# Optimization experiments

Hardware: AMD Instinct MI355X
Metric: run time of the kernel (lower is better)

Reference implementation:

```python
import jax, jax.numpy as jnp
import numpy as np

SAMPLING = 16   # VGG16 feature stride
POOL = 7        # adaptive max pool output size
KMAX = 5        # max bin window; valid for ROI feature extents <= 28 cells
NEG = jnp.float32(-1e30)


def _bin_bounds(s0, L, i):
    # torch AdaptiveMaxPool2d bin i over a length-L crop starting at s0:
    # [s0 + floor(i*L/P), s0 + ceil((i+1)*L/P))
    bs = s0 + (i * L) // POOL
    be = s0 + ((i + 1) * L + POOL - 1) // POOL
    return bs, be


def setup_inputs() -> dict:
    key = jax.random.key(0)
    ks = jax.random.split(key, 12)
    N, C, Hf, Wf = 1024, 512, 50, 84
    Himg, Wimg = Hf * SAMPLING, Wf * SAMPLING
    # post-ReLU VGG features -> non-negative
    featmap = jax.random.uniform(ks[0], (1, C, Hf, Wf), dtype=jnp.float32)
    # ROI boxes [x0, y0, x1, y1] in pixel coords, extents in [32, 448] px
    x0 = jax.random.randint(ks[1], (N,), 0, Wimg - 448)
    y0 = jax.random.randint(ks[2], (N,), 0, Himg - 448)
    w = jax.random.randint(ks[3], (N,), 32, 449)
    h = jax.random.randint(ks[4], (N,), 32, 449)
    roi = jnp.stack([x0, y0, x0 + w, y0 + h], axis=1).astype(jnp.int32)
    d = C * POOL * POOL  # 25088
    W1 = jax.random.normal(ks[5], (d, 4096), dtype=jnp.float32) * 0.01
    b1 = jnp.zeros((4096,), jnp.float32)
    W2 = jax.random.normal(ks[6], (4096, 4096), dtype=jnp.float32) * 0.01
    b2 = jnp.zeros((4096,), jnp.float32)
    Wc = jax.random.normal(ks[7], (4096, 3), dtype=jnp.float32) * 0.01
    bc = jnp.zeros((3,), jnp.float32)
    Wr = jax.random.normal(ks[8], (4096, 12), dtype=jnp.float32) * 0.01
    br = jnp.zeros((12,), jnp.float32)
    return {"featmap": featmap, "roi": roi, "W1": W1, "b1": b1, "W2": W2,
            "b2": b2, "Wc": Wc, "bc": bc, "Wr": Wr, "br": br}


def _roipool(featmap, roi):
    fm = featmap[0]                       # (C, Hf, Wf)
    C, Hf, Wf = fm.shape
    rf = roi // SAMPLING                  # floor, coords are non-negative
    x0, y0, x1, y1 = rf[:, 0], rf[:, 1], rf[:, 2], rf[:, 3]
    # width expand: if x1-x0 <= 1 -> grow right if in-bounds else grow left
    nw = (x1 - x0) <= 1
    x0n = jnp.where(nw & ~(x1 < Wf), x0 - 1, x0)
    x1n = jnp.where(nw & (x1 < Wf), x1 + 1, x1)
    nh = (y1 - y0) <= 1
    y0n = jnp.where(nh & ~(y1 < Hf), y0 - 1, y0)
    y1n = jnp.where(nh & (y1 < Hf), y1 + 1, y1)
    # python slice semantics clamp to array bounds
    xs, xe = jnp.clip(x0n, 0, Wf), jnp.clip(x1n, 0, Wf)
    ys, ye = jnp.clip(y0n, 0, Hf), jnp.clip(y1n, 0, Hf)
    Lx, Ly = xe - xs, ye - ys
    ar = jnp.arange(KMAX)
    rows = []
    for i in range(POOL):                 # fixed 7x7 bins
        hs, he = _bin_bounds(ys, Ly, i)
        h_idx = hs[:, None] + ar          # (N, K)
        h_ok = h_idx < he[:, None]
        h_idx = jnp.clip(h_idx, 0, Hf - 1)
        cols = []
        for j in range(POOL):
            ws_, we_ = _bin_bounds(xs, Lx, j)
            w_idx = ws_[:, None] + ar     # (N, K)
            w_ok = w_idx < we_[:, None]
            w_idx = jnp.clip(w_idx, 0, Wf - 1)
            patch = fm[:, h_idx[:, :, None], w_idx[:, None, :]]  # (C, N, K, K)
            m = h_ok[:, :, None] & w_ok[:, None, :]              # (N, K, K)
            patch = jnp.where(m[None], patch, NEG)
            cols.append(patch.max(axis=(2, 3)))                  # (C, N)
        rows.append(jnp.stack(cols, 0))   # (7, C, N)
    pool = jnp.stack(rows, 0)             # (7, 7, C, N)
    return pool.transpose(3, 2, 0, 1).reshape(roi.shape[0], -1)  # (N, C*49)


def reference(featmap, roi, W1, b1, W2, b2, Wc, bc, Wr, br):
    pooled = _roipool(featmap, roi)       # (N, 25088)
    h = (pooled @ W1 + b1) @ W2 + b2      # two Linears, no activation (as in source)
    output_cls = jax.nn.softmax(h @ Wc + bc, axis=1)
    output_reg = h @ Wr + br
    return output_cls, output_reg
```

## Files before the change

### kernel.cpp

```cpp
#include <hip/hip_runtime.h>
#include <hip/hip_bf16.h>
#include <cstdint>
#include <cstddef>

typedef __attribute__((ext_vector_type(4))) float f32x4;
typedef __attribute__((ext_vector_type(8))) short s16x8;
typedef __attribute__((ext_vector_type(4))) unsigned short u16x4;

__device__ __forceinline__ unsigned short f2bf(float f) {
    union { float f; unsigned u; } v; v.f = f;
    unsigned u = v.u;
    u += 0x7fffu + ((u >> 16) & 1u);
    return (unsigned short)(u >> 16);
}
__device__ __forceinline__ float lo_f(unsigned v) {
    union { unsigned u; float f; } w; w.u = v << 16; return w.f;
}
__device__ __forceinline__ float hi_f(unsigned v) {
    union { unsigned u; float f; } w; w.u = v & 0xffff0000u; return w.f;
}


__global__ __launch_bounds__(256) void prep_all(
        const float* __restrict__ fm, unsigned short* __restrict__ fmT,
        const float* __restrict__ Wc, const float* __restrict__ Wr,
        unsigned short* __restrict__ WcatT) {
    const int bid = blockIdx.x, t = threadIdx.x;
    if (bid < 2112) {
        __shared__ float tile[32][33];
        int p0 = (bid % 132) * 32, c0 = (bid / 132) * 32;
        int tx = t & 31, ty = t >> 5;
        #pragma unroll
        for (int yy = ty; yy < 32; yy += 8) {
            int p = p0 + tx;
            if (p < 4200) tile[yy][tx] = fm[(size_t)(c0 + yy) * 4200 + p];
        }
        __syncthreads();
        #pragma unroll
        for (int yy = ty; yy < 32; yy += 8) {
            int p = p0 + yy;
            if (p < 4200) fmT[(size_t)p * 512 + c0 + tx] = f2bf(tile[tx][yy]);
        }
    } else {
        int idx = (bid - 2112) * 256 + t;
        int i = idx >> 4, j = idx & 15;
        float v = (j < 3) ? Wc[i * 3 + j] : (j < 15) ? Wr[i * 12 + (j - 3)] : 0.f;
        WcatT[(size_t)j * 4096 + i] = f2bf(v);
    }
}

template<bool NT>
__device__ __forceinline__ void skinny_body(
        const float* __restrict__ A, const unsigned short* __restrict__ BT,
        float* __restrict__ partial, int R, int kchunk,
        int bx, int ky, int t) {
    const int lane = t & 63, wave = t >> 6;
    const int r0 = bx * 128 + wave * 16;
    const int k0 = ky * kchunk;
    const int lr = lane & 15, lks = lane >> 4;
    const int steps = kchunk >> 5;
    const float* ap = A + (size_t)(r0 + lr) * 4096 + k0 + lks * 8;
    const unsigned short* bp = BT + (size_t)lr * 4096 + k0 + lks * 8;
    f32x4 acc = {0.f, 0.f, 0.f, 0.f};
    for (int s = 0; s < steps; ++s) {
        f32x4 f0, f1;
        if (NT) {
            f0 = __builtin_nontemporal_load((const f32x4*)(ap + s * 32));
            f1 = __builtin_nontemporal_load((const f32x4*)(ap + s * 32 + 4));
        } else {
            f0 = *(const f32x4*)(ap + s * 32);
            f1 = *(const f32x4*)(ap + s * 32 + 4);
        }
        s16x8 b = *(const s16x8*)(bp + s * 32);
        union { unsigned short us[8]; s16x8 v; } a;
        a.us[0] = f2bf(f0.x); a.us[1] = f2bf(f0.y);
        a.us[2] = f2bf(f0.z); a.us[3] = f2bf(f0.w);
        a.us[4] = f2bf(f1.x); a.us[5] = f2bf(f1.y);
        a.us[6] = f2bf(f1.z); a.us[7] = f2bf(f1.w);
        acc = __builtin_amdgcn_mfma_f32_16x16x32_bf16(a.v, b, acc, 0, 0, 0);
    }
    const int row = r0 + (lane >> 4) * 4;
    float* op = partial + ((size_t)ky * R + row) * 16 + lr;
    #pragma unroll
    for (int q = 0; q < 4; ++q) {
        if (NT) __builtin_nontemporal_store(acc[q], op + q * 16);
        else    op[q * 16] = acc[q];
    }
}

__global__ __launch_bounds__(512) void skinny_w2(
        const float* __restrict__ W2, const unsigned short* __restrict__ WcatT,
        float* __restrict__ partial1) {
    skinny_body<false>(W2, WcatT, partial1, 4096, 512, blockIdx.x, blockIdx.y, threadIdx.x);
}

__global__ __launch_bounds__(256) void reduce_wf(
        const float* __restrict__ partial1, const float* __restrict__ b2,
        const float* __restrict__ Wc, const float* __restrict__ Wr,
        const float* __restrict__ bc, const float* __restrict__ br,
        float* __restrict__ Wf16, unsigned short* __restrict__ WfT,
        float* __restrict__ bfv) {
    const int t = threadIdx.x;
    if (blockIdx.x < 256) {
        int idx = blockIdx.x * 256 + t;
        float s = 0.f;
        #pragma unroll
        for (int sp = 0; sp < 8; ++sp) s += partial1[sp * 65536 + idx];
        Wf16[idx] = s;
        int i = idx >> 4, j = idx & 15;
        WfT[(size_t)j * 4096 + i] = f2bf(s);
    } else {
        float acc[15];
        #pragma unroll
        for (int j = 0; j < 15; ++j) acc[j] = 0.f;
        for (int i = t; i < 4096; i += 256) {
            float bv = b2[i];
            #pragma unroll
            for (int j = 0; j < 15; ++j)
                acc[j] += bv * ((j < 3) ? Wc[i * 3 + j] : Wr[i * 12 + (j - 3)]);
        }
        const int lane = t & 63, wv = t >> 6;
        __shared__ float red[4][15];
        #pragma unroll
        for (int j = 0; j < 15; ++j) {
            float x = acc[j];
            #pragma unroll
            for (int off = 32; off >= 1; off >>= 1) x += __shfl_xor(x, off, 64);
            if (lane == 0) red[wv][j] = x;
        }
        __syncthreads();
        if (t < 15)
            bfv[t] = red[0][t] + red[1][t] + red[2][t] + red[3][t]
                   + ((t < 3) ? bc[t] : br[t - 3]);
    }
}

#define PB(NH, NW) { \
    uint2 v[NH * NW]; \
    _Pragma("unroll") for (int r = 0; r < NH; ++r) \
        _Pragma("unroll") for (int s = 0; s < NW; ++s) \
            v[r * NW + s] = *(const uint2*)(base + ho[r] + wo[s]); \
    float a0 = lo_f(v[0].x), a1 = hi_f(v[0].x); \
    float a2 = lo_f(v[0].y), a3 = hi_f(v[0].y); \
    _Pragma("unroll") for (int q = 1; q < NH * NW; ++q) { \
        a0 = fmaxf(a0, lo_f(v[q].x)); a1 = fmaxf(a1, hi_f(v[q].x)); \
        a2 = fmaxf(a2, lo_f(v[q].y)); a3 = fmaxf(a3, hi_f(v[q].y)); } \
    m0 = a0; m1 = a1; m2 = a2; m3 = a3; } break;

__global__ __launch_bounds__(512) void megaB(
        const unsigned short* __restrict__ fmT, const int* __restrict__ roi,
        unsigned short* __restrict__ pooled,
        const float* __restrict__ W1, const unsigned short* __restrict__ WfT,
        float* __restrict__ partial2) {
    const int g7 = blockIdx.x / 7, r7 = blockIdx.x % 7;
    const int t = threadIdx.x;
    if (r7 < 3) {
        const int sb = g7 * 3 + r7;
        if (sb >= 784) return;
        const int ky = sb / 196, bx = sb % 196;
        skinny_body<true>(W1, WfT, partial2, 25088, 1024, bx, ky, t);
    } else {
        const int n = g7 * 4 + (r7 - 3);
        if (n >= 1024) return;
        __shared__ int hoff[7][5], woff[7][5], hcnt[7], wcnt[7];
        if (t == 0) {
            int x0 = roi[n*4+0] / 16, y0 = roi[n*4+1] / 16;
            int x1 = roi[n*4+2] / 16, y1 = roi[n*4+3] / 16;
            if (x1 - x0 <= 1) { if (x1 < 84) x1 += 1; else x0 -= 1; }
            if (y1 - y0 <= 1) { if (y1 < 50) y1 += 1; else y0 -= 1; }
            int xs = min(max(x0, 0), 84), xe = min(max(x1, 0), 84);
            int ys = min(max(y0, 0), 50), ye = min(max(y1, 0), 50);
            int Lx = xe - xs, Ly = ye - ys;
            #pragma unroll
            for (int i = 0; i < 7; ++i) {
                int b0 = ys + (i * Ly) / 7, b1 = ys + ((i + 1) * Ly + 6) / 7;
                hcnt[i] = min(b1, b0 + 5) - b0;
                int c0 = xs + (i * Lx) / 7, c1 = xs + ((i + 1) * Lx + 6) / 7;
                wcnt[i] = min(c1, c0 + 5) - c0;
                #pragma unroll
                for (int q = 0; q < 5; ++q) {
                    hoff[i][q] = (b0 + q) * 43008;
                    woff[i][q] = (c0 + q) * 512;
                }
            }
        }
        __syncthreads();
        const int g = t >> 7;
        const int c4 = (t & 127) * 4;
        const unsigned short* base = fmT + c4;
        unsigned short* orow = pooled + (size_t)n * 25088;
        for (int bp = 0; bp < 13; ++bp) {
            int bin = bp * 4 + g;
            if (bin < 49) {
                int bi = bin / 7, bj = bin - bi * 7;
                int ho[5], wo[5];
                #pragma unroll
                for (int q = 0; q < 5; ++q) { ho[q] = hoff[bi][q]; wo[q] = woff[bj][q]; }
                int nh = hcnt[bi], nw = wcnt[bj];
                float m0, m1, m2, m3;
                switch ((nh - 1) * 5 + (nw - 1)) {
                    case  0: PB(1,1)  case  1: PB(1,2)  case  2: PB(1,3)
                    case  3: PB(1,4)  case  4: PB(1,5)
                    case  5: PB(2,1)  case  6: PB(2,2)  case  7: PB(2,3)
                    case  8: PB(2,4)  case  9: PB(2,5)
                    case 10: PB(3,1)  case 11: PB(3,2)  case 12: PB(3,3)
                    case 13: PB(3,4)  case 14: PB(3,5)
                    case 15: PB(4,1)  case 16: PB(4,2)  case 17: PB(4,3)
                    case 18: PB(4,4)  case 19: PB(4,5)
                    case 20: PB(5,1)  case 21: PB(5,2)  case 22: PB(5,3)
                    case 23: PB(5,4)  case 24: PB(5,5)
                    default: m0 = m1 = m2 = m3 = 0.f; break;
                }
                u16x4 o;
                o.x = f2bf(m0); o.y = f2bf(m1); o.z = f2bf(m2); o.w = f2bf(m3);
                __builtin_nontemporal_store(o, (u16x4*)(orow + bin * 512 + c4));
            }
        }
    }
}

__global__ __launch_bounds__(256) void reduce_wbig(
        const float* __restrict__ partial2, const float* __restrict__ Wf16,
        const float* __restrict__ bfv, const float* __restrict__ b1,
        unsigned short* __restrict__ WbigT, float* __restrict__ bbig) {
    const int t = threadIdx.x;
    if (blockIdx.x < 98) {
        const int r = blockIdx.x * 256 + t;
        float sj[16];
        #pragma unroll
        for (int j = 0; j < 16; ++j) sj[j] = 0.f;
        #pragma unroll
        for (int sp = 0; sp < 4; ++sp) {
            const float4* pp = (const float4*)(partial2 + ((size_t)sp * 25088 + r) * 16);
            float4 a = pp[0], b = pp[1], c = pp[2], d = pp[3];
            sj[0] += a.x; sj[1] += a.y; sj[2]  += a.z; sj[3]  += a.w;
            sj[4] += b.x; sj[5] += b.y; sj[6]  += b.z; sj[7]  += b.w;
            sj[8] += c.x; sj[9] += c.y; sj[10] += c.z; sj[11] += c.w;
            sj[12] += d.x; sj[13] += d.y; sj[14] += d.z; sj[15] += d.w;
        }
        const int c = r / 49, bin = r - c * 49;
        const int p = bin * 512 + c;
        #pragma unroll
        for (int j = 0; j < 16; ++j)
            WbigT[(size_t)j * 25088 + p] = f2bf(sj[j]);
    } else {
        float acc[15];
        #pragma unroll
        for (int j = 0; j < 15; ++j) acc[j] = 0.f;
        for (int i = t; i < 4096; i += 256) {
            float bv = b1[i];
            #pragma unroll
            for (int j = 0; j < 15; ++j) acc[j] += bv * Wf16[i * 16 + j];
        }
        const int lane = t & 63, wv = t >> 6;
        __shared__ float red[4][15];
        #pragma unroll
        for (int j = 0; j < 15; ++j) {
            float x = acc[j];
            #pragma unroll
            for (int off = 32; off >= 1; off >>= 1) x += __shfl_xor(x, off, 64);
            if (lane == 0) red[wv][j] = x;
        }
        __syncthreads();
        if (t < 16) {
            float s = 0.f;
            if (t < 15)
                s = red[0][t] + red[1][t] + red[2][t] + red[3][t] + bfv[t];
            bbig[t] = s;
        }
    }
}

__global__ __launch_bounds__(256) void final_gemm(
        const unsigned short* __restrict__ pooled,
        const unsigned short* __restrict__ WbigT,
        float* __restrict__ partialG) {
    const int t = threadIdx.x, lane = t & 63, wave = t >> 6;
    const int m0 = blockIdx.x * 16, kz = blockIdx.y;
    const int lr = lane & 15, lks = lane >> 4;
    f32x4 acc = {0.f, 0.f, 0.f, 0.f};
    const unsigned short* arow = pooled + (size_t)(m0 + lr) * 25088 + kz * 3136 + lks * 8;
    const unsigned short* brow = WbigT + (size_t)lr * 25088 + kz * 3136 + lks * 8;
    for (int s = wave; s < 98; s += 4) {
        s16x8 a = __builtin_nontemporal_load((const s16x8*)(arow + s * 32));
        s16x8 b = *(const s16x8*)(brow + s * 32);
        acc = __builtin_amdgcn_mfma_f32_16x16x32_bf16(a, b, acc, 0, 0, 0);
    }
    __shared__ float red[4][64][4];
    #pragma unroll
    for (int r = 0; r < 4; ++r) red[wave][lane][r] = acc[r];
    __syncthreads();
    if (wave == 0) {
        #pragma unroll
        for (int r = 0; r < 4; ++r) {
            float s = red[0][lane][r] + red[1][lane][r] + red[2][lane][r] + red[3][lane][r];
            int row = m0 + (lane >> 4) * 4 + r;
            partialG[((size_t)kz * 1024 + row) * 16 + (lane & 15)] = s;
        }
    }
}

__global__ __launch_bounds__(256) void finalize_kernel(
        const float* __restrict__ partialG, const float* __restrict__ bbig,
        float* __restrict__ out) {
    const int m = blockIdx.x * 256 + threadIdx.x;
    float v[15];
    #pragma unroll
    for (int j = 0; j < 15; ++j) v[j] = bbig[j];
    for (int kz = 0; kz < 8; ++kz) {
        const float* p = partialG + ((size_t)kz * 1024 + m) * 16;
        #pragma unroll
        for (int j = 0; j < 15; ++j) v[j] += p[j];
    }
    float mx = fmaxf(v[0], fmaxf(v[1], v[2]));
    float e0 = expf(v[0] - mx), e1 = expf(v[1] - mx), e2 = expf(v[2] - mx);
    float inv = 1.f / (e0 + e1 + e2);
    out[m * 3 + 0] = e0 * inv;
    out[m * 3 + 1] = e1 * inv;
    out[m * 3 + 2] = e2 * inv;
    #pragma unroll
    for (int j = 3; j < 15; ++j) out[3072 + m * 12 + (j - 3)] = v[j];
}

extern "C" void kernel_launch(void* const* d_in, const int* in_sizes, int n_in,
                              void* d_out, int out_size, void* d_ws, size_t ws_size,
                              hipStream_t stream) {
    const float* featmap = (const float*)d_in[0];
    const int*   roi     = (const int*)d_in[1];
    const float* W1      = (const float*)d_in[2];
    const float* b1      = (const float*)d_in[3];
    const float* W2      = (const float*)d_in[4];
    const float* b2      = (const float*)d_in[5];
    const float* Wc      = (const float*)d_in[6];
    const float* bc      = (const float*)d_in[7];
    const float* Wr      = (const float*)d_in[8];
    const float* br      = (const float*)d_in[9];
    float* out = (float*)d_out;

    char* ws = (char*)d_ws;
    unsigned short* pooled   = (unsigned short*)(ws);
    unsigned short* fmT      = (unsigned short*)(ws + 51380224);
    unsigned short* WcatT    = (unsigned short*)(ws + 55681024);
    unsigned short* WfT      = (unsigned short*)(ws + 55812096);
    float*          Wf16     = (float*)        (ws + 55943168);
    float*          bfv      = (float*)        (ws + 56205312);
    float*          bbig     = (float*)        (ws + 56205376);
    float*          partial1 = (float*)        (ws + 56205440);
    float*          partial2 = (float*)        (ws + 60399744);
    unsigned short* WbigT    = (unsigned short*)(ws + 66822272);
    float*          partialG = (float*)        (ws + 67625088);

    prep_all<<<2368, 256, 0, stream>>>(featmap, fmT, Wc, Wr, WcatT);
    skinny_w2<<<dim3(32, 8), 512, 0, stream>>>(W2, WcatT, partial1);
    reduce_wf<<<257, 256, 0, stream>>>(partial1, b2, Wc, Wr, bc, br, Wf16, WfT, bfv);
    megaB<<<1834, 512, 0, stream>>>(fmT, roi, pooled, W1, WfT, partial2);
    reduce_wbig<<<99, 256, 0, stream>>>(partial2, Wf16, bfv, b1, WbigT, bbig);
    final_gemm<<<dim3(64, 8), 256, 0, stream>>>(pooled, WbigT, partialG);
    finalize_kernel<<<4, 256, 0, stream>>>(partialG, bbig, out);
}
```

Baseline: 220.3 us.

## Co-schedule featmap transpose with W2 skinny GEMM and split W1 K further

The featmap transpose moves out of the prep kernel and into the W2 skinny-GEMM kernel, interleaved one GEMM block per four transpose units, so the two independent jobs can overlap on the GPU. The Wc/Wr packing becomes its own small kernel that runs first. In megaB the W1 reduction's K chunk drops from 1024 to 512, doubling the split-K partitions to 8, and the block interleave shifts to three GEMM blocks per two ROI-pool blocks. This gives more parallelism on the large W1 streaming pass, at the cost of a larger partial buffer and more reduction traffic in reduce_wbig.

```diff
diff --git a/kernel.cpp b/kernel.cpp
--- a/kernel.cpp
+++ b/kernel.cpp
@@ -21,32 +21,13 @@
 }
 
 
-__global__ __launch_bounds__(256) void prep_all(
-        const float* __restrict__ fm, unsigned short* __restrict__ fmT,
+__global__ __launch_bounds__(256) void prep_wcat(
         const float* __restrict__ Wc, const float* __restrict__ Wr,
         unsigned short* __restrict__ WcatT) {
-    const int bid = blockIdx.x, t = threadIdx.x;
-    if (bid < 2112) {
-        __shared__ float tile[32][33];
-        int p0 = (bid % 132) * 32, c0 = (bid / 132) * 32;
-        int tx = t & 31, ty = t >> 5;
-        #pragma unroll
-        for (int yy = ty; yy < 32; yy += 8) {
-            int p = p0 + tx;
-            if (p < 4200) tile[yy][tx] = fm[(size_t)(c0 + yy) * 4200 + p];
-        }
-        __syncthreads();
-        #pragma unroll
-        for (int yy = ty; yy < 32; yy += 8) {
-            int p = p0 + yy;
-            if (p < 4200) fmT[(size_t)p * 512 + c0 + tx] = f2bf(tile[tx][yy]);
-        }
-    } else {
-        int idx = (bid - 2112) * 256 + t;
-        int i = idx >> 4, j = idx & 15;
-        float v = (j < 3) ? Wc[i * 3 + j] : (j < 15) ? Wr[i * 12 + (j - 3)] : 0.f;
-        WcatT[(size_t)j * 4096 + i] = f2bf(v);
-    }
+    int idx = blockIdx.x * 256 + threadIdx.x;
+    int i = idx >> 4, j = idx & 15;
+    float v = (j < 3) ? Wc[i * 3 + j] : (j < 15) ? Wr[i * 12 + (j - 3)] : 0.f;
+    WcatT[(size_t)j * 4096 + i] = f2bf(v);
 }
 
 template<bool NT>
@@ -88,10 +69,36 @@
     }
 }
 
-__global__ __launch_bounds__(512) void skinny_w2(
+__global__ __launch_bounds__(512) void prepA(
+        const float* __restrict__ fm, unsigned short* __restrict__ fmT,
         const float* __restrict__ W2, const unsigned short* __restrict__ WcatT,
         float* __restrict__ partial1) {
-    skinny_body<false>(W2, WcatT, partial1, 4096, 512, blockIdx.x, blockIdx.y, threadIdx.x);
+    const int g5 = blockIdx.x / 5, r5 = blockIdx.x % 5;
+    const int t = threadIdx.x;
+    if (r5 < 4) {
+        const int unit = g5 * 4 + r5;
+        if (unit >= 1056) return;
+        __shared__ float tile[2][32][33];
+        const int sub = t >> 8, tt = t & 255;
+        const int tid = unit * 2 + sub;
+        const int p0 = (tid % 132) * 32, c0 = (tid / 132) * 32;
+        const int tx = tt & 31, ty = tt >> 5;
+        #pragma unroll
+        for (int yy = ty; yy < 32; yy += 8) {
+            int p = p0 + tx;
+            if (p < 4200) tile[sub][yy][tx] = fm[(size_t)(c0 + yy) * 4200 + p];
+        }
+        __syncthreads();
+        #pragma unroll
+        for (int yy = ty; yy < 32; yy += 8) {
+            int p = p0 + yy;
+            if (p < 4200) fmT[(size_t)p * 512 + c0 + tx] = f2bf(tile[sub][tx][yy]);
+        }
+    } else {
+        const int v = g5;
+        if (v >= 256) return;
+        skinny_body<false>(W2, WcatT, partial1, 4096, 512, v & 31, v >> 5, t);
+    }
 }
 
 __global__ __launch_bounds__(256) void reduce_wf(
@@ -152,15 +159,15 @@
         unsigned short* __restrict__ pooled,
         const float* __restrict__ W1, const unsigned short* __restrict__ WfT,
         float* __restrict__ partial2) {
-    const int g7 = blockIdx.x / 7, r7 = blockIdx.x % 7;
+    const int g5 = blockIdx.x / 5, r5 = blockIdx.x % 5;
     const int t = threadIdx.x;
-    if (r7 < 3) {
-        const int sb = g7 * 3 + r7;
-        if (sb >= 784) return;
+    if (r5 < 3) {
+        const int sb = g5 * 3 + r5;
+        if (sb >= 1568) return;
         const int ky = sb / 196, bx = sb % 196;
-        skinny_body<true>(W1, WfT, partial2, 25088, 1024, bx, ky, t);
+        skinny_body<true>(W1, WfT, partial2, 25088, 512, bx, ky, t);
     } else {
-        const int n = g7 * 4 + (r7 - 3);
+        const int n = g5 * 2 + (r5 - 3);
         if (n >= 1024) return;
         __shared__ int hoff[7][5], woff[7][5], hcnt[7], wcnt[7];
         if (t == 0) {
@@ -230,7 +237,7 @@
         #pragma unroll
         for (int j = 0; j < 16; ++j) sj[j] = 0.f;
         #pragma unroll
-        for (int sp = 0; sp < 4; ++sp) {
+        for (int sp = 0; sp < 8; ++sp) {
             const float4* pp = (const float4*)(partial2 + ((size_t)sp * 25088 + r) * 16);
             float4 a = pp[0], b = pp[1], c = pp[2], d = pp[3];
             sj[0] += a.x; sj[1] += a.y; sj[2]  += a.z; sj[3]  += a.w;
@@ -347,13 +354,13 @@
     float*          bbig     = (float*)        (ws + 56205376);
     float*          partial1 = (float*)        (ws + 56205440);
     float*          partial2 = (float*)        (ws + 60399744);
-    unsigned short* WbigT    = (unsigned short*)(ws + 66822272);
-    float*          partialG = (float*)        (ws + 67625088);
-
-    prep_all<<<2368, 256, 0, stream>>>(featmap, fmT, Wc, Wr, WcatT);
-    skinny_w2<<<dim3(32, 8), 512, 0, stream>>>(W2, WcatT, partial1);
+    unsigned short* WbigT    = (unsigned short*)(ws + 111779968);
+    float*          partialG = (float*)        (ws + 112582784);
+
+    prep_wcat<<<256, 256, 0, stream>>>(Wc, Wr, WcatT);
+    prepA<<<1320, 512, 0, stream>>>(featmap, fmT, W2, WcatT, partial1);
     reduce_wf<<<257, 256, 0, stream>>>(partial1, b2, Wc, Wr, bc, br, Wf16, WfT, bfv);
-    megaB<<<1834, 512, 0, stream>>>(fmT, roi, pooled, W1, WfT, partial2);
+    megaB<<<2615, 512, 0, stream>>>(fmT, roi, pooled, W1, WfT, partial2);
     reduce_wbig<<<99, 256, 0, stream>>>(partial2, Wf16, bfv, b1, WbigT, bbig);
     final_gemm<<<dim3(64, 8), 256, 0, stream>>>(pooled, WbigT, partialG);
     finalize_kernel<<<4, 256, 0, stream>>>(partialG, bbig, out);
```

After: 214.4 us (median of 2 runs). 1.03x faster.
